# Performance work log

Measured on AMD Instinct MI355X. Metric: run time of the kernel, lower is better.

The kernel has to match this reference:

```python
import jax, jax.numpy as jnp
import numpy as np

N_NODES = 100000
D = 128


def _sage_layer(h, src, dst, w_self, w_neigh, b):
    # GraphSAGE mean aggregation: mean of neighbor (src) features per dst node.
    msg = h[src]                                            # [E, D] gather
    agg = jax.ops.segment_sum(msg, dst, num_segments=N_NODES)  # [N, D]
    deg = jax.ops.segment_sum(jnp.ones(src.shape, h.dtype), dst, num_segments=N_NODES)
    mean = agg / jnp.maximum(deg, 1.0)[:, None]
    return h @ w_self + mean @ w_neigh + b


def setup_inputs() -> dict:
    key = jax.random.key(0)
    ks = jax.random.split(key, 16)
    E = 1600000
    inp = {
        "feat": jax.random.normal(ks[0], (N_NODES, D), jnp.float32),
        "edge0_src": jax.random.randint(ks[1], (E,), 0, N_NODES),
        "edge0_dst": jax.random.randint(ks[2], (E,), 0, N_NODES),
        "edge1_src": jax.random.randint(ks[3], (E,), 0, N_NODES),
        "edge1_dst": jax.random.randint(ks[4], (E,), 0, N_NODES),
        "pos_src": jax.random.randint(ks[5], (100000,), 0, N_NODES),
        "pos_dst": jax.random.randint(ks[6], (100000,), 0, N_NODES),
        "neg_src": jax.random.randint(ks[7], (500000,), 0, N_NODES),
        "neg_dst": jax.random.randint(ks[8], (500000,), 0, N_NODES),
        # learned parameters
        "w_proj": jax.random.normal(ks[9], (D, D), jnp.float32) / np.sqrt(D),
        "b_proj": jnp.zeros((D,), jnp.float32),
        "w_self1": jax.random.normal(ks[10], (D, D), jnp.float32) / np.sqrt(D),
        "w_neigh1": jax.random.normal(ks[11], (D, D), jnp.float32) / np.sqrt(D),
        "b1": jnp.zeros((D,), jnp.float32),
        "w_self2": jax.random.normal(ks[12], (D, D), jnp.float32) / np.sqrt(D),
        "w_neigh2": jax.random.normal(ks[13], (D, D), jnp.float32) / np.sqrt(D),
        "b2": jnp.zeros((D,), jnp.float32),
    }
    return inp


def reference(feat, edge0_src, edge0_dst, edge1_src, edge1_dst,
              pos_src, pos_dst, neg_src, neg_dst,
              w_proj, b_proj, w_self1, w_neigh1, b1, w_self2, w_neigh2, b2):
    # ProjectionLayer: per-node linear + ReLU on blocks[0].srcdata['feature']
    h = jax.nn.relu(feat @ w_proj + b_proj)
    # GNNLayer: one SAGE-mean layer per block
    h = jax.nn.relu(_sage_layer(h, edge0_src, edge0_dst, w_self1, w_neigh1, b1))
    h = _sage_layer(h, edge1_src, edge1_dst, w_self2, w_neigh2, b2)
    # PredictionLayer: dot-product edge scoring on pos_graph / neg_graph
    pos_score = jnp.sum(h[pos_src] * h[pos_dst], axis=-1)
    neg_score = jnp.sum(h[neg_src] * h[neg_dst], axis=-1)
    return (pos_score, neg_score)
```

## Files before the change

### kernel.cpp

```cpp
#include <hip/hip_runtime.h>
#include <hip/hip_bf16.h>

#define NN 100000
#define DD 128

#define NPB 512
#define NB 196
#define CAPB 12288
#define PA_BLOCKS 196
#define GBLK 782

typedef unsigned short ushort_t;
typedef unsigned int uint_t;
typedef __attribute__((ext_vector_type(8))) short bf16x8;
typedef __attribute__((ext_vector_type(4))) float f32x4;

__device__ __forceinline__ ushort_t f2bf(float f) {
    uint_t u = __builtin_bit_cast(uint_t, f);
    u += 0x7FFFu + ((u >> 16) & 1u);
    return (ushort_t)(u >> 16);
}
__device__ __forceinline__ uint_t pack2bf(float a, float b) {
    return (uint_t)f2bf(a) | ((uint_t)f2bf(b) << 16);
}
__device__ __forceinline__ float bflo(uint_t v) {
    return __builtin_bit_cast(float, v << 16);
}
__device__ __forceinline__ float bfhi(uint_t v) {
    return __builtin_bit_cast(float, v & 0xFFFF0000u);
}

__device__ __forceinline__ void gload16(const ushort_t* g, ushort_t* l) {
    __builtin_amdgcn_global_load_lds(
        (const __attribute__((address_space(1))) void*)g,
        (__attribute__((address_space(3))) void*)l,
        16, 0, 0);
}

#define PREP_W_BLOCKS 320
#define PREP_Z_BLOCKS 3
__global__ __launch_bounds__(256) void prep(
    const float* __restrict__ w_proj,
    const float* __restrict__ w_self1, const float* __restrict__ w_neigh1,
    const float* __restrict__ w_self2, const float* __restrict__ w_neigh2,
    ushort_t* __restrict__ wtp, ushort_t* __restrict__ wt1,
    ushort_t* __restrict__ wt2, int* __restrict__ bcnt,
    ushort_t* __restrict__ h1pad, ushort_t* __restrict__ h2pad)
{
    const int bid = blockIdx.x;
    const int tid = threadIdx.x;
    if (bid < PREP_W_BLOCKS) {
        int which = bid >> 6;
        int t = (bid & 63) * 256 + tid;
        int n = t >> 7, k = t & 127;
        float v;
        ushort_t* d;
        switch (which) {
            case 0: v = w_proj  [(size_t)k * 128 + n]; d = wtp + (size_t)n * 128 + k;       break;
            case 1: v = w_self1 [(size_t)k * 128 + n]; d = wt1 + (size_t)n * 256 + k;       break;
            case 2: v = w_neigh1[(size_t)k * 128 + n]; d = wt1 + (size_t)n * 256 + 128 + k; break;
            case 3: v = w_self2 [(size_t)k * 128 + n]; d = wt2 + (size_t)n * 256 + k;       break;
            default:v = w_neigh2[(size_t)k * 128 + n]; d = wt2 + (size_t)n * 256 + 128 + k; break;
        }
        *d = f2bf(v);
    } else if (bid < PREP_W_BLOCKS + 2) {
        int i = (bid - PREP_W_BLOCKS) * 256 + tid;
        if (i < 2 * NB) bcnt[i] = 0;
    } else {
        uint_t* p1 = (uint_t*)h1pad;
        uint_t* p2 = (uint_t*)h2pad;
        if (tid < 64) p1[tid] = 0;
        else if (tid < 128) p2[tid - 64] = 0;
    }
}

__global__ __launch_bounds__(256, 4) void gemm0_partA2(
    const float* __restrict__ feat, const ushort_t* __restrict__ W,
    const float* __restrict__ bias, ushort_t* __restrict__ outp,
    const int* __restrict__ e0s, const int* __restrict__ e0d, int E0,
    const int* __restrict__ e1s, const int* __restrict__ e1d, int E1,
    int* __restrict__ bcnt, uint_t* __restrict__ pairs)
{
    __shared__ char smem[32768];
    const int tid = threadIdx.x;

    if (blockIdx.x < GBLK) {
        ushort_t* At = (ushort_t*)smem;
        ushort_t* Wt = (ushort_t*)(smem + 8192);
        ushort_t* Ot = (ushort_t*)smem;

        const int lane = tid & 63;
        const int wav  = tid >> 6;
        const int row0 = blockIdx.x * 128;
        const int m0   = (wav & 1) * 64;
        const int n0   = (wav >> 1) * 64;

        f32x4 acc[4][4];
#pragma unroll
        for (int i = 0; i < 4; ++i)
#pragma unroll
            for (int j = 0; j < 4; ++j) acc[i][j] = (f32x4){0.f, 0.f, 0.f, 0.f};

        const int cl = lane & 15;
        const int q  = lane >> 4;

#pragma unroll 1
        for (int ch = 0; ch < 4; ++ch) {
            const int kA = ch * 32;

            if (ch) __syncthreads();
#pragma unroll
            for (int j = 0; j < 2; ++j) {
                int cb = (j * 4 + wav) * 64;
                int c  = cb + lane;
                int r  = c >> 2, k2 = c & 3;
                gload16(W + (size_t)r * 128 + kA + k2 * 8, Wt + cb * 8);
            }
            uint4 av[2];
#pragma unroll
            for (int j = 0; j < 2; ++j) {
                int g = tid + 256 * j;
                int r = g >> 2;
                int c = (g & 3) * 8;
                int grow = row0 + r;
                if (grow >= NN) grow = NN - 1;
                float4 f0 = *(const float4*)(feat + (size_t)grow * DD + kA + c);
                float4 f1 = *(const float4*)(feat + (size_t)grow * DD + kA + c + 4);
                av[j].x = pack2bf(f0.x, f0.y);
                av[j].y = pack2bf(f0.z, f0.w);
                av[j].z = pack2bf(f1.x, f1.y);
                av[j].w = pack2bf(f1.z, f1.w);
            }
#pragma unroll
            for (int j = 0; j < 2; ++j) {
                int g = tid + 256 * j;
                int r = g >> 2;
                int c = (g & 3) * 8;
                *(uint4*)(&At[r * 32 + c]) = av[j];
            }
            __syncthreads();

            bf16x8 af[4], bfr[4];
#pragma unroll
            for (int i = 0; i < 4; ++i)
                af[i] = *(const bf16x8*)(&At[(m0 + i * 16 + cl) * 32 + q * 8]);
#pragma unroll
            for (int j = 0; j < 4; ++j)
                bfr[j] = *(const bf16x8*)(&Wt[(n0 + j * 16 + cl) * 32 + q * 8]);
#pragma unroll
            for (int i = 0; i < 4; ++i)
#pragma unroll
                for (int j = 0; j < 4; ++j)
                    acc[i][j] = __builtin_amdgcn_mfma_f32_16x16x32_bf16(
                        af[i], bfr[j], acc[i][j], 0, 0, 0);
        }

        __syncthreads();
#pragma unroll
        for (int j = 0; j < 4; ++j) {
            int c = n0 + j * 16 + cl;
            float bv = bias[c];
#pragma unroll
            for (int i = 0; i < 4; ++i) {
#pragma unroll
                for (int reg = 0; reg < 4; ++reg) {
                    int r = m0 + i * 16 + 4 * q + reg;
                    float v = acc[i][j][reg] + bv;
                    v = fmaxf(v, 0.f);
                    Ot[r * 128 + c] = f2bf(v);
                }
            }
        }
        __syncthreads();
        int rows = NN - row0; if (rows > 128) rows = 128;
        for (int t = tid; t < rows * 16; t += 256) {
            int r = t >> 4, c8 = (t & 15) * 8;
            *(uint4*)(outp + (size_t)(row0 + r) * DD + c8) =
                *(const uint4*)(&Ot[r * 128 + c8]);
        }
    } else {
        int* hist = (int*)smem;
        int* base = (int*)(smem + 1024);

        const int bid  = blockIdx.x - GBLK;
        const int half = bid >= PA_BLOCKS;
        const int* __restrict__ src = half ? e1s : e0s;
        const int* __restrict__ dst = half ? e1d : e0d;
        const int E = half ? E1 : E0;
        int* bc = bcnt + half * NB;
        uint_t* pp = pairs + (size_t)half * NB * CAPB;
        const int blk = bid - half * PA_BLOCKS;
        const int chunk = (E + PA_BLOCKS - 1) / PA_BLOCKS;
        const int ea = blk * chunk;
        int eb = ea + chunk; if (eb > E) eb = E;

        for (int b = tid; b < NB; b += 256) hist[b] = 0;
        __syncthreads();
        for (int e = ea + tid; e < eb; e += 256)
            atomicAdd(&hist[dst[e] >> 9], 1);
        __syncthreads();
        for (int b = tid; b < NB; b += 256) {
            base[b] = atomicAdd(&bc[b], hist[b]);
            hist[b] = 0;
        }
        __syncthreads();
        for (int e = ea + tid; e < eb; e += 256) {
            int d = dst[e];
            int b = d >> 9;
            int off = atomicAdd(&hist[b], 1);
            int p = base[b] + off;
            if (p < CAPB)
                pp[(size_t)b * CAPB + p] =
                    ((uint_t)(d & (NPB - 1)) << 17) | (uint_t)src[e];
        }
    }
}

template <bool RELU>
__global__ __launch_bounds__(256, 4) void gemm_bf16(
    const ushort_t* __restrict__ Av, const ushort_t* __restrict__ Bm,
    const ushort_t* __restrict__ W, const float* __restrict__ bias,
    ushort_t* __restrict__ outp)
{
    __shared__ char smem[32768];
    ushort_t* Ot = (ushort_t*)smem;

    const int tid  = threadIdx.x;
    const int lane = tid & 63;
    const int wav  = tid >> 6;
    const int row0 = blockIdx.x * 128;
    const int m0   = (wav & 1) * 64;
    const int n0   = (wav >> 1) * 64;
    const int KTOT = 256;
    const int NCH  = 8;

    f32x4 acc[4][4];
#pragma unroll
    for (int i = 0; i < 4; ++i)
#pragma unroll
        for (int j = 0; j < 4; ++j) acc[i][j] = (f32x4){0.f, 0.f, 0.f, 0.f};

    const int cl = lane & 15;
    const int q  = lane >> 4;

    auto STAGE = [&](int ch, int buf) {
        const bool second = (ch >= 4);
        const int kA = (ch & 3) * 32;
        const int kW = ch * 32;
        ushort_t* At = (ushort_t*)(smem + buf * 16384);
        ushort_t* Wt = At + 4096;
        const ushort_t* sp = second ? Bm : Av;
#pragma unroll
        for (int j = 0; j < 2; ++j) {
            int cb = (j * 4 + wav) * 64;
            int c  = cb + lane;
            int r  = c >> 2, k2 = c & 3;
            int grow = row0 + r;
            if (grow >= NN) grow = NN - 1;
            gload16(sp + (size_t)grow * DD + kA + k2 * 8, At + cb * 8);
            gload16(W + (size_t)r * KTOT + kW + k2 * 8, Wt + cb * 8);
        }
    };
    auto COMPUTE = [&](int buf) {
        ushort_t* At = (ushort_t*)(smem + buf * 16384);
        ushort_t* Wt = At + 4096;
        bf16x8 af[4], bfr[4];
#pragma unroll
        for (int i = 0; i < 4; ++i)
            af[i] = *(const bf16x8*)(&At[(m0 + i * 16 + cl) * 32 + q * 8]);
#pragma unroll
        for (int j = 0; j < 4; ++j)
            bfr[j] = *(const bf16x8*)(&Wt[(n0 + j * 16 + cl) * 32 + q * 8]);
#pragma unroll
        for (int i = 0; i < 4; ++i)
#pragma unroll
            for (int j = 0; j < 4; ++j)
                acc[i][j] = __builtin_amdgcn_mfma_f32_16x16x32_bf16(
                    af[i], bfr[j], acc[i][j], 0, 0, 0);
    };

    STAGE(0, 0);
    asm volatile("s_waitcnt vmcnt(0)" ::: "memory");
    __builtin_amdgcn_s_barrier();
    int cur = 0;
#pragma unroll 1
    for (int ch = 0; ch < NCH - 1; ++ch) {
        STAGE(ch + 1, cur ^ 1);
        COMPUTE(cur);
        asm volatile("s_waitcnt vmcnt(0)" ::: "memory");
        __builtin_amdgcn_s_barrier();
        cur ^= 1;
    }
    COMPUTE(cur);

    __syncthreads();
#pragma unroll
    for (int j = 0; j < 4; ++j) {
        int c = n0 + j * 16 + cl;
        float bv = bias[c];
#pragma unroll
        for (int i = 0; i < 4; ++i) {
#pragma unroll
            for (int reg = 0; reg < 4; ++reg) {
                int r = m0 + i * 16 + 4 * q + reg;
                float v = acc[i][j][reg] + bv;
                if constexpr (RELU) v = fmaxf(v, 0.f);
                Ot[r * 128 + c] = f2bf(v);
            }
        }
    }
    __syncthreads();
    int rows = NN - row0; if (rows > 128) rows = 128;
    for (int t = tid; t < rows * 16; t += 256) {
        int r = t >> 4, c8 = (t & 15) * 8;
        *(uint4*)(outp + (size_t)(row0 + r) * DD + c8) =
            *(const uint4*)(&Ot[r * 128 + c8]);
    }
}

__global__ __launch_bounds__(256, 2) void partB(
    uint_t* __restrict__ pairs, const int* __restrict__ bcnt,
    int* __restrict__ counts, int* __restrict__ offs)
{
    __shared__ int cnt[NPB];
    __shared__ int loff[NPB];
    __shared__ int ssc[256];
    __shared__ int image[CAPB];

    const int tid  = threadIdx.x;
    const int half = blockIdx.x >= NB;
    const int b    = blockIdx.x - half * NB;
    const int n0   = b << 9;
    int nb = NN - n0; if (nb > NPB) nb = NPB;
    int tot = bcnt[half * NB + b]; if (tot > CAPB) tot = CAPB;
    uint_t* pb = pairs + (size_t)(half * NB + b) * CAPB;
    const int gbase = (half * NB + b) * CAPB;
    int* cnts  = counts + (size_t)half * NN;
    int* offsl = offs   + (size_t)half * NN;

    for (int n = tid; n < NPB; n += 256) cnt[n] = 0;
    __syncthreads();
    for (int i = tid; i < tot; i += 256)
        atomicAdd(&cnt[pb[i] >> 17], 1);
    __syncthreads();

    int a0 = cnt[2 * tid], a1 = cnt[2 * tid + 1];
    int s = a0 + a1;
    ssc[tid] = s;
    __syncthreads();
    for (int off = 1; off < 256; off <<= 1) {
        int t = 0;
        if (tid >= off) t = ssc[tid - off];
        __syncthreads();
        if (tid >= off) ssc[tid] += t;
        __syncthreads();
    }
    int pre = ssc[tid] - s;
    loff[2 * tid]     = pre;
    loff[2 * tid + 1] = pre + a0;
    __syncthreads();

    for (int n = tid; n < nb; n += 256) {
        cnts[n0 + n]  = cnt[n];
        offsl[n0 + n] = gbase + loff[n];
    }
    for (int n = tid; n < NPB; n += 256) cnt[n] = 0;
    __syncthreads();

    for (int i = tid; i < tot; i += 256) {
        uint_t p = pb[i];
        int ln  = p >> 17;
        int pos = loff[ln] + atomicAdd(&cnt[ln], 1);
        image[pos] = (int)(p & 0x1FFFFu);
    }
    __syncthreads();
    for (int i = tid; i < tot; i += 256) pb[i] = (uint_t)image[i];
}

#define AGG_ISSUE(V, J)                                                   \
    do {                                                                  \
        int s_[8];                                                        \
        _Pragma("unroll")                                                 \
        for (int u = 0; u < 8; ++u) {                                     \
            int jj = (J) + u;                                             \
            int jc = jj < cnt ? jj : cnt - 1;                             \
            int sv = (int)csr[start + jc];                                \
            s_[u] = jj < cnt ? sv : NN;                                   \
        }                                                                 \
        _Pragma("unroll")                                                 \
        for (int u = 0; u < 8; ++u)                                       \
            V[u] = *(const uint4*)(hl + (size_t)s_[u] * DD);              \
    } while (0)

#define AGG_ACCUM(V)                                                      \
    do {                                                                  \
        _Pragma("unroll")                                                 \
        for (int u = 0; u < 8; ++u) {                                     \
            a0 += bflo(V[u].x); a1 += bfhi(V[u].x);                       \
            a2 += bflo(V[u].y); a3 += bfhi(V[u].y);                       \
            a4 += bflo(V[u].z); a5 += bfhi(V[u].z);                       \
            a6 += bflo(V[u].w); a7 += bfhi(V[u].w);                       \
        }                                                                 \
    } while (0)

__global__ __launch_bounds__(256) void aggregate_bf16(
    const ushort_t* __restrict__ h, const uint_t* __restrict__ csr,
    const int* __restrict__ offs, const int* __restrict__ counts,
    ushort_t* __restrict__ mean, int nn)
{
    int gid  = blockIdx.x * 256 + threadIdx.x;
    int node = gid >> 4;
    if (node >= nn) return;
    int lane  = gid & 15;
    int start = offs[node];
    int cnt   = counts[node];
    const ushort_t* __restrict__ hl = h + lane * 8;

    float a0 = 0.f, a1 = 0.f, a2 = 0.f, a3 = 0.f;
    float a4 = 0.f, a5 = 0.f, a6 = 0.f, a7 = 0.f;

    int nbt = (cnt + 7) >> 3;
    if (nbt > 0) {
        uint4 va[8], vb[8];
        AGG_ISSUE(va, 0);
        int j = 8, b = 1;
        for (; b + 1 < nbt; b += 2) {
            AGG_ISSUE(vb, j); j += 8;
            AGG_ACCUM(va);
            AGG_ISSUE(va, j); j += 8;
            AGG_ACCUM(vb);
        }
        if (b < nbt) {
            AGG_ISSUE(vb, j);
            AGG_ACCUM(va);
            AGG_ACCUM(vb);
        } else {
            AGG_ACCUM(va);
        }
    }

    float rinv = 1.0f / (float)(cnt > 1 ? cnt : 1);
    uint4 o;
    o.x = pack2bf(a0 * rinv, a1 * rinv);
    o.y = pack2bf(a2 * rinv, a3 * rinv);
    o.z = pack2bf(a4 * rinv, a5 * rinv);
    o.w = pack2bf(a6 * rinv, a7 * rinv);
    *(uint4*)(mean + (size_t)node * DD + lane * 8) = o;
}

__device__ __forceinline__ float dot8(uint4 a, uint4 b) {
    return bflo(a.x) * bflo(b.x) + bfhi(a.x) * bfhi(b.x)
         + bflo(a.y) * bflo(b.y) + bfhi(a.y) * bfhi(b.y)
         + bflo(a.z) * bflo(b.z) + bfhi(a.z) * bfhi(b.z)
         + bflo(a.w) * bflo(b.w) + bfhi(a.w) * bfhi(b.w);
}

__global__ __launch_bounds__(256) void score_both(
    const ushort_t* __restrict__ h,
    const int* __restrict__ ps, const int* __restrict__ pd,
    const int* __restrict__ ns, const int* __restrict__ nd,
    float* __restrict__ out, int EP, int TE)
{
    int gid = blockIdx.x * 256 + threadIdx.x;
    int grp = gid >> 4;
    int e0 = grp * 2;
    if (e0 >= TE) return;
    int lane = gid & 15;
    int e1 = e0 + 1;
    bool has1 = (e1 < TE);
    int ee = has1 ? e1 : e0;

    int s0, d0, s1, d1;
    if (e0 < EP) { s0 = ps[e0]; d0 = pd[e0]; }
    else         { s0 = ns[e0 - EP]; d0 = nd[e0 - EP]; }
    if (ee < EP) { s1 = ps[ee]; d1 = pd[ee]; }
    else         { s1 = ns[ee - EP]; d1 = nd[ee - EP]; }

    const ushort_t* __restrict__ hl = h + lane * 8;
    uint4 va0 = *(const uint4*)(hl + (size_t)s0 * DD);
    uint4 vb0 = *(const uint4*)(hl + (size_t)d0 * DD);
    uint4 va1 = *(const uint4*)(hl + (size_t)s1 * DD);
    uint4 vb1 = *(const uint4*)(hl + (size_t)d1 * DD);

    float r0 = dot8(va0, vb0);
    float r1 = dot8(va1, vb1);
#pragma unroll
    for (int off = 8; off; off >>= 1) {
        r0 += __shfl_down(r0, off, 16);
        r1 += __shfl_down(r1, off, 16);
    }
    if (lane == 0) {
        out[e0] = r0;
        if (has1) out[e1] = r1;
    }
}


extern "C" void kernel_launch(void* const* d_in, const int* in_sizes, int n_in,
                              void* d_out, int out_size, void* d_ws, size_t ws_size,
                              hipStream_t stream)
{
    const float* feat    = (const float*)d_in[0];
    const int*   e0s     = (const int*)d_in[1];
    const int*   e0d     = (const int*)d_in[2];
    const int*   e1s     = (const int*)d_in[3];
    const int*   e1d     = (const int*)d_in[4];
    const int*   ps      = (const int*)d_in[5];
    const int*   pd      = (const int*)d_in[6];
    const int*   ns      = (const int*)d_in[7];
    const int*   nd      = (const int*)d_in[8];
    const float* w_proj  = (const float*)d_in[9];
    const float* b_proj  = (const float*)d_in[10];
    const float* w_self1 = (const float*)d_in[11];
    const float* w_neigh1= (const float*)d_in[12];
    const float* b1      = (const float*)d_in[13];
    const float* w_self2 = (const float*)d_in[14];
    const float* w_neigh2= (const float*)d_in[15];
    const float* b2      = (const float*)d_in[16];

    float* out = (float*)d_out;

    const size_t NF  = (size_t)NN * DD;
    const size_t NFP = NF + DD;
    char* base = (char*)d_ws;

    ushort_t* h3   = (ushort_t*)base;
    ushort_t* h1   = h3 + NFP;
    ushort_t* mean = h1 + NFP;
    ushort_t* h2   = mean + NFP;

    uint_t* pairs  = (uint_t*)(h2 + NFP);
    int*    bcnt   = (int*)(pairs + (size_t)2 * NB * CAPB);
    int*    counts = bcnt + 2 * NB;
    int*    offs   = counts + 2 * NN;
    ushort_t* wts  = (ushort_t*)(offs + 2 * NN);
    ushort_t* wtp = wts;
    ushort_t* wt1 = wts + 128 * 128;
    ushort_t* wt2 = wt1 + 128 * 256;

    const int E0 = in_sizes[1];
    const int E1 = in_sizes[3];
    const int EP = in_sizes[5];
    const int EN = in_sizes[7];

    const int AGB = (NN * 16 + 255) / 256;

    prep<<<PREP_W_BLOCKS + PREP_Z_BLOCKS, 256, 0, stream>>>(
        w_proj, w_self1, w_neigh1, w_self2, w_neigh2, wtp, wt1, wt2, bcnt,
        h1 + NF, h2 + NF);

    gemm0_partA2<<<GBLK + 2 * PA_BLOCKS, 256, 0, stream>>>(
        feat, wtp, b_proj, h1, e0s, e0d, E0, e1s, e1d, E1, bcnt, pairs);

    partB<<<2 * NB, 256, 0, stream>>>(pairs, bcnt, counts, offs);

    aggregate_bf16<<<AGB, 256, 0, stream>>>(h1, pairs, offs, counts, mean, NN);
    gemm_bf16<true><<<GBLK, 256, 0, stream>>>(h1, mean, wt1, b1, h2);

    aggregate_bf16<<<AGB, 256, 0, stream>>>(
        h2, pairs, offs + NN, counts + NN, mean, NN);
    gemm_bf16<false><<<GBLK, 256, 0, stream>>>(h2, mean, wt2, b2, h3);

    const int TE = EP + EN;
    const int NG = (TE + 1) / 2;
    score_both<<<(NG * 16 + 255) / 256, 256, 0, stream>>>(
        h3, ps, pd, ns, nd, out, EP, TE);
}
```

Before: 402.7 us.

## Fuse neighbor mean aggregation into SAGE layer GEMM via shared-memory mean tile

Each SAGE layer now runs as one kernel. Every 128-row block first gathers and averages neighbor features for its nodes into a padded shared-memory tile, then runs the concatenated self/neighbor GEMM using that tile directly. This removes the global round trip of the mean buffer and two kernel launches. The projection GEMM and edge bucketing are also split back into separate kernels. In exchange, the GEMM loses its double-buffered staging, shared memory per block rises to about 50KB, and occupancy is capped at 3 blocks, so gather latency can no longer be hidden by as many resident waves.

```diff
diff --git a/kernel.cpp b/kernel.cpp
--- a/kernel.cpp
+++ b/kernel.cpp
@@ -74,155 +74,13 @@
     }
 }
 
-__global__ __launch_bounds__(256, 4) void gemm0_partA2(
+__global__ __launch_bounds__(256, 4) void gemm0(
     const float* __restrict__ feat, const ushort_t* __restrict__ W,
-    const float* __restrict__ bias, ushort_t* __restrict__ outp,
-    const int* __restrict__ e0s, const int* __restrict__ e0d, int E0,
-    const int* __restrict__ e1s, const int* __restrict__ e1d, int E1,
-    int* __restrict__ bcnt, uint_t* __restrict__ pairs)
+    const float* __restrict__ bias, ushort_t* __restrict__ outp)
 {
     __shared__ char smem[32768];
-    const int tid = threadIdx.x;
-
-    if (blockIdx.x < GBLK) {
-        ushort_t* At = (ushort_t*)smem;
-        ushort_t* Wt = (ushort_t*)(smem + 8192);
-        ushort_t* Ot = (ushort_t*)smem;
-
-        const int lane = tid & 63;
-        const int wav  = tid >> 6;
-        const int row0 = blockIdx.x * 128;
-        const int m0   = (wav & 1) * 64;
-        const int n0   = (wav >> 1) * 64;
-
-        f32x4 acc[4][4];
-#pragma unroll
-        for (int i = 0; i < 4; ++i)
-#pragma unroll
-            for (int j = 0; j < 4; ++j) acc[i][j] = (f32x4){0.f, 0.f, 0.f, 0.f};
-
-        const int cl = lane & 15;
-        const int q  = lane >> 4;
-
-#pragma unroll 1
-        for (int ch = 0; ch < 4; ++ch) {
-            const int kA = ch * 32;
-
-            if (ch) __syncthreads();
-#pragma unroll
-            for (int j = 0; j < 2; ++j) {
-                int cb = (j * 4 + wav) * 64;
-                int c  = cb + lane;
-                int r  = c >> 2, k2 = c & 3;
-                gload16(W + (size_t)r * 128 + kA + k2 * 8, Wt + cb * 8);
-            }
-            uint4 av[2];
-#pragma unroll
-            for (int j = 0; j < 2; ++j) {
-                int g = tid + 256 * j;
-                int r = g >> 2;
-                int c = (g & 3) * 8;
-                int grow = row0 + r;
-                if (grow >= NN) grow = NN - 1;
-                float4 f0 = *(const float4*)(feat + (size_t)grow * DD + kA + c);
-                float4 f1 = *(const float4*)(feat + (size_t)grow * DD + kA + c + 4);
-                av[j].x = pack2bf(f0.x, f0.y);
-                av[j].y = pack2bf(f0.z, f0.w);
-                av[j].z = pack2bf(f1.x, f1.y);
-                av[j].w = pack2bf(f1.z, f1.w);
-            }
-#pragma unroll
-            for (int j = 0; j < 2; ++j) {
-                int g = tid + 256 * j;
-                int r = g >> 2;
-                int c = (g & 3) * 8;
-                *(uint4*)(&At[r * 32 + c]) = av[j];
-            }
-            __syncthreads();
-
-            bf16x8 af[4], bfr[4];
-#pragma unroll
-            for (int i = 0; i < 4; ++i)
-                af[i] = *(const bf16x8*)(&At[(m0 + i * 16 + cl) * 32 + q * 8]);
-#pragma unroll
-            for (int j = 0; j < 4; ++j)
-                bfr[j] = *(const bf16x8*)(&Wt[(n0 + j * 16 + cl) * 32 + q * 8]);
-#pragma unroll
-            for (int i = 0; i < 4; ++i)
-#pragma unroll
-                for (int j = 0; j < 4; ++j)
-                    acc[i][j] = __builtin_amdgcn_mfma_f32_16x16x32_bf16(
-                        af[i], bfr[j], acc[i][j], 0, 0, 0);
-        }
-
-        __syncthreads();
-#pragma unroll
-        for (int j = 0; j < 4; ++j) {
-            int c = n0 + j * 16 + cl;
-            float bv = bias[c];
-#pragma unroll
-            for (int i = 0; i < 4; ++i) {
-#pragma unroll
-                for (int reg = 0; reg < 4; ++reg) {
-                    int r = m0 + i * 16 + 4 * q + reg;
-                    float v = acc[i][j][reg] + bv;
-                    v = fmaxf(v, 0.f);
-                    Ot[r * 128 + c] = f2bf(v);
-                }
-            }
-        }
-        __syncthreads();
-        int rows = NN - row0; if (rows > 128) rows = 128;
-        for (int t = tid; t < rows * 16; t += 256) {
-            int r = t >> 4, c8 = (t & 15) * 8;
-            *(uint4*)(outp + (size_t)(row0 + r) * DD + c8) =
-                *(const uint4*)(&Ot[r * 128 + c8]);
-        }
-    } else {
-        int* hist = (int*)smem;
-        int* base = (int*)(smem + 1024);
-
-        const int bid  = blockIdx.x - GBLK;
-        const int half = bid >= PA_BLOCKS;
-        const int* __restrict__ src = half ? e1s : e0s;
-        const int* __restrict__ dst = half ? e1d : e0d;
-        const int E = half ? E1 : E0;
-        int* bc = bcnt + half * NB;
-        uint_t* pp = pairs + (size_t)half * NB * CAPB;
-        const int blk = bid - half * PA_BLOCKS;
-        const int chunk = (E + PA_BLOCKS - 1) / PA_BLOCKS;
-        const int ea = blk * chunk;
-        int eb = ea + chunk; if (eb > E) eb = E;
-
-        for (int b = tid; b < NB; b += 256) hist[b] = 0;
-        __syncthreads();
-        for (int e = ea + tid; e < eb; e += 256)
-            atomicAdd(&hist[dst[e] >> 9], 1);
-        __syncthreads();
-        for (int b = tid; b < NB; b += 256) {
-            base[b] = atomicAdd(&bc[b], hist[b]);
-            hist[b] = 0;
-        }
-        __syncthreads();
-        for (int e = ea + tid; e < eb; e += 256) {
-            int d = dst[e];
-            int b = d >> 9;
-            int off = atomicAdd(&hist[b], 1);
-            int p = base[b] + off;
-            if (p < CAPB)
-                pp[(size_t)b * CAPB + p] =
-                    ((uint_t)(d & (NPB - 1)) << 17) | (uint_t)src[e];
-        }
-    }
-}
-
-template <bool RELU>
-__global__ __launch_bounds__(256, 4) void gemm_bf16(
-    const ushort_t* __restrict__ Av, const ushort_t* __restrict__ Bm,
-    const ushort_t* __restrict__ W, const float* __restrict__ bias,
-    ushort_t* __restrict__ outp)
-{
-    __shared__ char smem[32768];
+    ushort_t* At = (ushort_t*)smem;
+    ushort_t* Wt = (ushort_t*)(smem + 8192);
     ushort_t* Ot = (ushort_t*)smem;
 
     const int tid  = threadIdx.x;
@@ -231,8 +89,6 @@
     const int row0 = blockIdx.x * 128;
     const int m0   = (wav & 1) * 64;
     const int n0   = (wav >> 1) * 64;
-    const int KTOT = 256;
-    const int NCH  = 8;
 
     f32x4 acc[4][4];
 #pragma unroll
@@ -243,27 +99,42 @@
     const int cl = lane & 15;
     const int q  = lane >> 4;
 
-    auto STAGE = [&](int ch, int buf) {
-        const bool second = (ch >= 4);
-        const int kA = (ch & 3) * 32;
-        const int kW = ch * 32;
-        ushort_t* At = (ushort_t*)(smem + buf * 16384);
-        ushort_t* Wt = At + 4096;
-        const ushort_t* sp = second ? Bm : Av;
+#pragma unroll 1
+    for (int ch = 0; ch < 4; ++ch) {
+        const int kA = ch * 32;
+
+        if (ch) __syncthreads();
 #pragma unroll
         for (int j = 0; j < 2; ++j) {
             int cb = (j * 4 + wav) * 64;
             int c  = cb + lane;
             int r  = c >> 2, k2 = c & 3;
+            gload16(W + (size_t)r * 128 + kA + k2 * 8, Wt + cb * 8);
+        }
+        uint4 av[2];
+#pragma unroll
+        for (int j = 0; j < 2; ++j) {
+            int g = tid + 256 * j;
+            int r = g >> 2;
+            int c = (g & 3) * 8;
             int grow = row0 + r;
             if (grow >= NN) grow = NN - 1;
-            gload16(sp + (size_t)grow * DD + kA + k2 * 8, At + cb * 8);
-            gload16(W + (size_t)r * KTOT + kW + k2 * 8, Wt + cb * 8);
-        }
-    };
-    auto COMPUTE = [&](int buf) {
-        ushort_t* At = (ushort_t*)(smem + buf * 16384);
-        ushort_t* Wt = At + 4096;
+            float4 f0 = *(const float4*)(feat + (size_t)grow * DD + kA + c);
+            float4 f1 = *(const float4*)(feat + (size_t)grow * DD + kA + c + 4);
+            av[j].x = pack2bf(f0.x, f0.y);
+            av[j].y = pack2bf(f0.z, f0.w);
+            av[j].z = pack2bf(f1.x, f1.y);
+            av[j].w = pack2bf(f1.z, f1.w);
+        }
+#pragma unroll
+        for (int j = 0; j < 2; ++j) {
+            int g = tid + 256 * j;
+            int r = g >> 2;
+            int c = (g & 3) * 8;
+            *(uint4*)(&At[r * 32 + c]) = av[j];
+        }
+        __syncthreads();
+
         bf16x8 af[4], bfr[4];
 #pragma unroll
         for (int i = 0; i < 4; ++i)
@@ -277,21 +148,7 @@
             for (int j = 0; j < 4; ++j)
                 acc[i][j] = __builtin_amdgcn_mfma_f32_16x16x32_bf16(
                     af[i], bfr[j], acc[i][j], 0, 0, 0);
-    };
-
-    STAGE(0, 0);
-    asm volatile("s_waitcnt vmcnt(0)" ::: "memory");
-    __builtin_amdgcn_s_barrier();
-    int cur = 0;
-#pragma unroll 1
-    for (int ch = 0; ch < NCH - 1; ++ch) {
-        STAGE(ch + 1, cur ^ 1);
-        COMPUTE(cur);
-        asm volatile("s_waitcnt vmcnt(0)" ::: "memory");
-        __builtin_amdgcn_s_barrier();
-        cur ^= 1;
-    }
-    COMPUTE(cur);
+    }
 
     __syncthreads();
 #pragma unroll
@@ -304,7 +161,7 @@
             for (int reg = 0; reg < 4; ++reg) {
                 int r = m0 + i * 16 + 4 * q + reg;
                 float v = acc[i][j][reg] + bv;
-                if constexpr (RELU) v = fmaxf(v, 0.f);
+                v = fmaxf(v, 0.f);
                 Ot[r * 128 + c] = f2bf(v);
             }
         }
@@ -315,6 +172,46 @@
         int r = t >> 4, c8 = (t & 15) * 8;
         *(uint4*)(outp + (size_t)(row0 + r) * DD + c8) =
             *(const uint4*)(&Ot[r * 128 + c8]);
+    }
+}
+
+__global__ __launch_bounds__(256) void partA2(
+    const int* __restrict__ e0s, const int* __restrict__ e0d, int E0,
+    const int* __restrict__ e1s, const int* __restrict__ e1d, int E1,
+    int* __restrict__ bcnt, uint_t* __restrict__ pairs)
+{
+    __shared__ int hist[NB];
+    __shared__ int base[NB];
+    const int tid  = threadIdx.x;
+    const int half = blockIdx.x >= PA_BLOCKS;
+    const int* __restrict__ src = half ? e1s : e0s;
+    const int* __restrict__ dst = half ? e1d : e0d;
+    const int E = half ? E1 : E0;
+    int* bc = bcnt + half * NB;
+    uint_t* pp = pairs + (size_t)half * NB * CAPB;
+    const int blk = blockIdx.x - half * PA_BLOCKS;
+    const int chunk = (E + PA_BLOCKS - 1) / PA_BLOCKS;
+    const int ea = blk * chunk;
+    int eb = ea + chunk; if (eb > E) eb = E;
+
+    for (int b = tid; b < NB; b += 256) hist[b] = 0;
+    __syncthreads();
+    for (int e = ea + tid; e < eb; e += 256)
+        atomicAdd(&hist[dst[e] >> 9], 1);
+    __syncthreads();
+    for (int b = tid; b < NB; b += 256) {
+        base[b] = atomicAdd(&bc[b], hist[b]);
+        hist[b] = 0;
+    }
+    __syncthreads();
+    for (int e = ea + tid; e < eb; e += 256) {
+        int d = dst[e];
+        int b = d >> 9;
+        int off = atomicAdd(&hist[b], 1);
+        int p = base[b] + off;
+        if (p < CAPB)
+            pp[(size_t)b * CAPB + p] =
+                ((uint_t)(d & (NPB - 1)) << 17) | (uint_t)src[e];
     }
 }
 
@@ -403,49 +300,163 @@
         }                                                                 \
     } while (0)
 
-__global__ __launch_bounds__(256) void aggregate_bf16(
-    const ushort_t* __restrict__ h, const uint_t* __restrict__ csr,
+template <bool RELU>
+__global__ __launch_bounds__(256, 3) void fused_layer(
+    const ushort_t* __restrict__ hin, const uint_t* __restrict__ csr,
     const int* __restrict__ offs, const int* __restrict__ counts,
-    ushort_t* __restrict__ mean, int nn)
-{
-    int gid  = blockIdx.x * 256 + threadIdx.x;
-    int node = gid >> 4;
-    if (node >= nn) return;
-    int lane  = gid & 15;
-    int start = offs[node];
-    int cnt   = counts[node];
-    const ushort_t* __restrict__ hl = h + lane * 8;
-
-    float a0 = 0.f, a1 = 0.f, a2 = 0.f, a3 = 0.f;
-    float a4 = 0.f, a5 = 0.f, a6 = 0.f, a7 = 0.f;
-
-    int nbt = (cnt + 7) >> 3;
-    if (nbt > 0) {
-        uint4 va[8], vb[8];
-        AGG_ISSUE(va, 0);
-        int j = 8, b = 1;
-        for (; b + 1 < nbt; b += 2) {
-            AGG_ISSUE(vb, j); j += 8;
-            AGG_ACCUM(va);
-            AGG_ISSUE(va, j); j += 8;
-            AGG_ACCUM(vb);
-        }
-        if (b < nbt) {
-            AGG_ISSUE(vb, j);
-            AGG_ACCUM(va);
-            AGG_ACCUM(vb);
-        } else {
-            AGG_ACCUM(va);
-        }
-    }
-
-    float rinv = 1.0f / (float)(cnt > 1 ? cnt : 1);
-    uint4 o;
-    o.x = pack2bf(a0 * rinv, a1 * rinv);
-    o.y = pack2bf(a2 * rinv, a3 * rinv);
-    o.z = pack2bf(a4 * rinv, a5 * rinv);
-    o.w = pack2bf(a6 * rinv, a7 * rinv);
-    *(uint4*)(mean + (size_t)node * DD + lane * 8) = o;
+    const ushort_t* __restrict__ W, const float* __restrict__ bias,
+    ushort_t* __restrict__ outp)
+{
+    __shared__ char smem[51200];
+    ushort_t* Mean = (ushort_t*)smem;
+    ushort_t* Wt   = (ushort_t*)(smem + 34816);
+    ushort_t* At   = (ushort_t*)(smem + 43008);
+    ushort_t* Ot   = (ushort_t*)smem;
+
+    const int tid  = threadIdx.x;
+    const int row0 = blockIdx.x * 128;
+
+    {
+        const int grp    = tid >> 4;
+        const int lane16 = tid & 15;
+        const ushort_t* __restrict__ hl = hin + lane16 * 8;
+#pragma unroll 1
+        for (int g = 0; g < 8; ++g) {
+            int nloc = g * 16 + grp;
+            int node = row0 + nloc;
+            if (node >= NN) node = NN - 1;
+            int start = offs[node];
+            int cnt   = counts[node];
+
+            float a0 = 0.f, a1 = 0.f, a2 = 0.f, a3 = 0.f;
+            float a4 = 0.f, a5 = 0.f, a6 = 0.f, a7 = 0.f;
+            int nbt = (cnt + 7) >> 3;
+            if (nbt > 0) {
+                uint4 va[8], vb[8];
+                AGG_ISSUE(va, 0);
+                int j = 8, b = 1;
+                for (; b + 1 < nbt; b += 2) {
+                    AGG_ISSUE(vb, j); j += 8;
+                    AGG_ACCUM(va);
+                    AGG_ISSUE(va, j); j += 8;
+                    AGG_ACCUM(vb);
+                }
+                if (b < nbt) {
+                    AGG_ISSUE(vb, j);
+                    AGG_ACCUM(va);
+                    AGG_ACCUM(vb);
+                } else {
+                    AGG_ACCUM(va);
+                }
+            }
+            float rinv = 1.0f / (float)(cnt > 1 ? cnt : 1);
+            uint4 o;
+            o.x = pack2bf(a0 * rinv, a1 * rinv);
+            o.y = pack2bf(a2 * rinv, a3 * rinv);
+            o.z = pack2bf(a4 * rinv, a5 * rinv);
+            o.w = pack2bf(a6 * rinv, a7 * rinv);
+            *(uint4*)(&Mean[nloc * 136 + lane16 * 8]) = o;
+        }
+    }
+
+    const int lane = tid & 63;
+    const int wav  = tid >> 6;
+    const int m0   = (wav & 1) * 64;
+    const int n0   = (wav >> 1) * 64;
+    const int cl   = lane & 15;
+    const int q    = lane >> 4;
+
+    f32x4 acc[4][4];
+#pragma unroll
+    for (int i = 0; i < 4; ++i)
+#pragma unroll
+        for (int j = 0; j < 4; ++j) acc[i][j] = (f32x4){0.f, 0.f, 0.f, 0.f};
+
+    __syncthreads();
+
+#pragma unroll 1
+    for (int ch = 4; ch < 8; ++ch) {
+        const int kA = (ch & 3) * 32;
+        const int kW = ch * 32;
+        if (ch > 4) __syncthreads();
+#pragma unroll
+        for (int j = 0; j < 2; ++j) {
+            int cb = (j * 4 + wav) * 64;
+            int c  = cb + lane;
+            int r  = c >> 2, k2 = c & 3;
+            gload16(W + (size_t)r * 256 + kW + k2 * 8, Wt + cb * 8);
+        }
+        __syncthreads();
+
+        bf16x8 af[4], bfr[4];
+#pragma unroll
+        for (int i = 0; i < 4; ++i)
+            af[i] = *(const bf16x8*)(&Mean[(m0 + i * 16 + cl) * 136 + kA + q * 8]);
+#pragma unroll
+        for (int j = 0; j < 4; ++j)
+            bfr[j] = *(const bf16x8*)(&Wt[(n0 + j * 16 + cl) * 32 + q * 8]);
+#pragma unroll
+        for (int i = 0; i < 4; ++i)
+#pragma unroll
+            for (int j = 0; j < 4; ++j)
+                acc[i][j] = __builtin_amdgcn_mfma_f32_16x16x32_bf16(
+                    af[i], bfr[j], acc[i][j], 0, 0, 0);
+    }
+
+#pragma unroll 1
+    for (int ch = 0; ch < 4; ++ch) {
+        const int kA = ch * 32;
+        __syncthreads();
+#pragma unroll
+        for (int j = 0; j < 2; ++j) {
+            int cb = (j * 4 + wav) * 64;
+            int c  = cb + lane;
+            int r  = c >> 2, k2 = c & 3;
+            int grow = row0 + r;
+            if (grow >= NN) grow = NN - 1;
+            gload16(hin + (size_t)grow * DD + kA + k2 * 8, At + cb * 8);
+            gload16(W + (size_t)r * 256 + kA + k2 * 8, Wt + cb * 8);
+        }
+        __syncthreads();
+
+        bf16x8 af[4], bfr[4];
+#pragma unroll
+        for (int i = 0; i < 4; ++i)
+            af[i] = *(const bf16x8*)(&At[(m0 + i * 16 + cl) * 32 + q * 8]);
+#pragma unroll
+        for (int j = 0; j < 4; ++j)
+            bfr[j] = *(const bf16x8*)(&Wt[(n0 + j * 16 + cl) * 32 + q * 8]);
+#pragma unroll
+        for (int i = 0; i < 4; ++i)
+#pragma unroll
+            for (int j = 0; j < 4; ++j)
+                acc[i][j] = __builtin_amdgcn_mfma_f32_16x16x32_bf16(
+                    af[i], bfr[j], acc[i][j], 0, 0, 0);
+    }
+
+    __syncthreads();
+#pragma unroll
+    for (int j = 0; j < 4; ++j) {
+        int c = n0 + j * 16 + cl;
+        float bv = bias[c];
+#pragma unroll
+        for (int i = 0; i < 4; ++i) {
+#pragma unroll
+            for (int reg = 0; reg < 4; ++reg) {
+                int r = m0 + i * 16 + 4 * q + reg;
+                float v = acc[i][j][reg] + bv;
+                if constexpr (RELU) v = fmaxf(v, 0.f);
+                Ot[r * 128 + c] = f2bf(v);
+            }
+        }
+    }
+    __syncthreads();
+    int rows = NN - row0; if (rows > 128) rows = 128;
+    for (int t = tid; t < rows * 16; t += 256) {
+        int r = t >> 4, c8 = (t & 15) * 8;
+        *(uint4*)(outp + (size_t)(row0 + r) * DD + c8) =
+            *(const uint4*)(&Ot[r * 128 + c8]);
+    }
 }
 
 __device__ __forceinline__ float dot8(uint4 a, uint4 b) {
@@ -543,23 +554,21 @@
     const int EP = in_sizes[5];
     const int EN = in_sizes[7];
 
-    const int AGB = (NN * 16 + 255) / 256;
-
     prep<<<PREP_W_BLOCKS + PREP_Z_BLOCKS, 256, 0, stream>>>(
         w_proj, w_self1, w_neigh1, w_self2, w_neigh2, wtp, wt1, wt2, bcnt,
         h1 + NF, h2 + NF);
 
-    gemm0_partA2<<<GBLK + 2 * PA_BLOCKS, 256, 0, stream>>>(
-        feat, wtp, b_proj, h1, e0s, e0d, E0, e1s, e1d, E1, bcnt, pairs);
-
+    partA2<<<2 * PA_BLOCKS, 256, 0, stream>>>(
+        e0s, e0d, E0, e1s, e1d, E1, bcnt, pairs);
     partB<<<2 * NB, 256, 0, stream>>>(pairs, bcnt, counts, offs);
 
-    aggregate_bf16<<<AGB, 256, 0, stream>>>(h1, pairs, offs, counts, mean, NN);
-    gemm_bf16<true><<<GBLK, 256, 0, stream>>>(h1, mean, wt1, b1, h2);
-
-    aggregate_bf16<<<AGB, 256, 0, stream>>>(
-        h2, pairs, offs + NN, counts + NN, mean, NN);
-    gemm_bf16<false><<<GBLK, 256, 0, stream>>>(h2, mean, wt2, b2, h3);
+    gemm0<<<GBLK, 256, 0, stream>>>(feat, wtp, b_proj, h1);
+
+    fused_layer<true><<<GBLK, 256, 0, stream>>>(
+        h1, pairs, offs, counts, wt1, b1, h2);
+
+    fused_layer<false><<<GBLK, 256, 0, stream>>>(
+        h2, pairs, offs + NN, counts + NN, wt2, b2, h3);
 
     const int TE = EP + EN;
     const int NG = (TE + 1) / 2;
```

Result: slower. 422.5 us (+4.9%).

## Split fused projection GEMM and edge bucketing into separate kernels with 512-thread blocks

Applied to the files above, without the earlier changes.

The combined gemm0_partA2 launch is split into a standalone projection GEMM and a standalone edge-bucketing kernel. partA2 and partB now run with 512-thread blocks, and partB's scan works on one element per thread. The projection GEMM is launched after partB so the bucketing work no longer shares a grid with the GEMM. This trades the overlap that came from fusing the two jobs for simpler, better-occupied kernels, at the cost of an extra kernel launch.

```diff
diff --git a/kernel.cpp b/kernel.cpp
--- a/kernel.cpp
+++ b/kernel.cpp
@@ -74,146 +74,201 @@
     }
 }
 
-__global__ __launch_bounds__(256, 4) void gemm0_partA2(
+__global__ __launch_bounds__(256, 4) void gemm0(
     const float* __restrict__ feat, const ushort_t* __restrict__ W,
-    const float* __restrict__ bias, ushort_t* __restrict__ outp,
+    const float* __restrict__ bias, ushort_t* __restrict__ outp)
+{
+    __shared__ char smem[32768];
+    ushort_t* At = (ushort_t*)smem;
+    ushort_t* Wt = (ushort_t*)(smem + 8192);
+    ushort_t* Ot = (ushort_t*)smem;
+
+    const int tid  = threadIdx.x;
+    const int lane = tid & 63;
+    const int wav  = tid >> 6;
+    const int row0 = blockIdx.x * 128;
+    const int m0   = (wav & 1) * 64;
+    const int n0   = (wav >> 1) * 64;
+
+    f32x4 acc[4][4];
+#pragma unroll
+    for (int i = 0; i < 4; ++i)
+#pragma unroll
+        for (int j = 0; j < 4; ++j) acc[i][j] = (f32x4){0.f, 0.f, 0.f, 0.f};
+
+    const int cl = lane & 15;
+    const int q  = lane >> 4;
+
+#pragma unroll 1
+    for (int ch = 0; ch < 4; ++ch) {
+        const int kA = ch * 32;
+
+        if (ch) __syncthreads();
+#pragma unroll
+        for (int j = 0; j < 2; ++j) {
+            int cb = (j * 4 + wav) * 64;
+            int c  = cb + lane;
+            int r  = c >> 2, k2 = c & 3;
+            gload16(W + (size_t)r * 128 + kA + k2 * 8, Wt + cb * 8);
+        }
+        uint4 av[2];
+#pragma unroll
+        for (int j = 0; j < 2; ++j) {
+            int g = tid + 256 * j;
+            int r = g >> 2;
+            int c = (g & 3) * 8;
+            int grow = row0 + r;
+            if (grow >= NN) grow = NN - 1;
+            float4 f0 = *(const float4*)(feat + (size_t)grow * DD + kA + c);
+            float4 f1 = *(const float4*)(feat + (size_t)grow * DD + kA + c + 4);
+            av[j].x = pack2bf(f0.x, f0.y);
+            av[j].y = pack2bf(f0.z, f0.w);
+            av[j].z = pack2bf(f1.x, f1.y);
+            av[j].w = pack2bf(f1.z, f1.w);
+        }
+#pragma unroll
+        for (int j = 0; j < 2; ++j) {
+            int g = tid + 256 * j;
+            int r = g >> 2;
+            int c = (g & 3) * 8;
+            *(uint4*)(&At[r * 32 + c]) = av[j];
+        }
+        __syncthreads();
+
+        bf16x8 af[4], bfr[4];
+#pragma unroll
+        for (int i = 0; i < 4; ++i)
+            af[i] = *(const bf16x8*)(&At[(m0 + i * 16 + cl) * 32 + q * 8]);
+#pragma unroll
+        for (int j = 0; j < 4; ++j)
+            bfr[j] = *(const bf16x8*)(&Wt[(n0 + j * 16 + cl) * 32 + q * 8]);
+#pragma unroll
+        for (int i = 0; i < 4; ++i)
+#pragma unroll
+            for (int j = 0; j < 4; ++j)
+                acc[i][j] = __builtin_amdgcn_mfma_f32_16x16x32_bf16(
+                    af[i], bfr[j], acc[i][j], 0, 0, 0);
+    }
+
+    __syncthreads();
+#pragma unroll
+    for (int j = 0; j < 4; ++j) {
+        int c = n0 + j * 16 + cl;
+        float bv = bias[c];
+#pragma unroll
+        for (int i = 0; i < 4; ++i) {
+#pragma unroll
+            for (int reg = 0; reg < 4; ++reg) {
+                int r = m0 + i * 16 + 4 * q + reg;
+                float v = acc[i][j][reg] + bv;
+                v = fmaxf(v, 0.f);
+                Ot[r * 128 + c] = f2bf(v);
+            }
+        }
+    }
+    __syncthreads();
+    int rows = NN - row0; if (rows > 128) rows = 128;
+    for (int t = tid; t < rows * 16; t += 256) {
+        int r = t >> 4, c8 = (t & 15) * 8;
+        *(uint4*)(outp + (size_t)(row0 + r) * DD + c8) =
+            *(const uint4*)(&Ot[r * 128 + c8]);
+    }
+}
+
+__global__ __launch_bounds__(512) void partA2(
     const int* __restrict__ e0s, const int* __restrict__ e0d, int E0,
     const int* __restrict__ e1s, const int* __restrict__ e1d, int E1,
     int* __restrict__ bcnt, uint_t* __restrict__ pairs)
 {
-    __shared__ char smem[32768];
-    const int tid = threadIdx.x;
-
-    if (blockIdx.x < GBLK) {
-        ushort_t* At = (ushort_t*)smem;
-        ushort_t* Wt = (ushort_t*)(smem + 8192);
-        ushort_t* Ot = (ushort_t*)smem;
-
-        const int lane = tid & 63;
-        const int wav  = tid >> 6;
-        const int row0 = blockIdx.x * 128;
-        const int m0   = (wav & 1) * 64;
-        const int n0   = (wav >> 1) * 64;
-
-        f32x4 acc[4][4];
-#pragma unroll
-        for (int i = 0; i < 4; ++i)
-#pragma unroll
-            for (int j = 0; j < 4; ++j) acc[i][j] = (f32x4){0.f, 0.f, 0.f, 0.f};
-
-        const int cl = lane & 15;
-        const int q  = lane >> 4;
-
-#pragma unroll 1
-        for (int ch = 0; ch < 4; ++ch) {
-            const int kA = ch * 32;
-
-            if (ch) __syncthreads();
-#pragma unroll
-            for (int j = 0; j < 2; ++j) {
-                int cb = (j * 4 + wav) * 64;
-                int c  = cb + lane;
-                int r  = c >> 2, k2 = c & 3;
-                gload16(W + (size_t)r * 128 + kA + k2 * 8, Wt + cb * 8);
-            }
-            uint4 av[2];
-#pragma unroll
-            for (int j = 0; j < 2; ++j) {
-                int g = tid + 256 * j;
-                int r = g >> 2;
-                int c = (g & 3) * 8;
-                int grow = row0 + r;
-                if (grow >= NN) grow = NN - 1;
-                float4 f0 = *(const float4*)(feat + (size_t)grow * DD + kA + c);
-                float4 f1 = *(const float4*)(feat + (size_t)grow * DD + kA + c + 4);
-                av[j].x = pack2bf(f0.x, f0.y);
-                av[j].y = pack2bf(f0.z, f0.w);
-                av[j].z = pack2bf(f1.x, f1.y);
-                av[j].w = pack2bf(f1.z, f1.w);
-            }
-#pragma unroll
-            for (int j = 0; j < 2; ++j) {
-                int g = tid + 256 * j;
-                int r = g >> 2;
-                int c = (g & 3) * 8;
-                *(uint4*)(&At[r * 32 + c]) = av[j];
-            }
-            __syncthreads();
-
-            bf16x8 af[4], bfr[4];
-#pragma unroll
-            for (int i = 0; i < 4; ++i)
-                af[i] = *(const bf16x8*)(&At[(m0 + i * 16 + cl) * 32 + q * 8]);
-#pragma unroll
-            for (int j = 0; j < 4; ++j)
-                bfr[j] = *(const bf16x8*)(&Wt[(n0 + j * 16 + cl) * 32 + q * 8]);
-#pragma unroll
-            for (int i = 0; i < 4; ++i)
-#pragma unroll
-                for (int j = 0; j < 4; ++j)
-                    acc[i][j] = __builtin_amdgcn_mfma_f32_16x16x32_bf16(
-                        af[i], bfr[j], acc[i][j], 0, 0, 0);
-        }
-
+    __shared__ int hist[NB];
+    __shared__ int base[NB];
+    const int tid  = threadIdx.x;
+    const int half = blockIdx.x >= PA_BLOCKS;
+    const int* __restrict__ src = half ? e1s : e0s;
+    const int* __restrict__ dst = half ? e1d : e0d;
+    const int E = half ? E1 : E0;
+    int* bc = bcnt + half * NB;
+    uint_t* pp = pairs + (size_t)half * NB * CAPB;
+    const int blk = blockIdx.x - half * PA_BLOCKS;
+    const int chunk = (E + PA_BLOCKS - 1) / PA_BLOCKS;
+    const int ea = blk * chunk;
+    int eb = ea + chunk; if (eb > E) eb = E;
+
+    for (int b = tid; b < NB; b += 512) hist[b] = 0;
+    __syncthreads();
+    for (int e = ea + tid; e < eb; e += 512)
+        atomicAdd(&hist[dst[e] >> 9], 1);
+    __syncthreads();
+    for (int b = tid; b < NB; b += 512) {
+        base[b] = atomicAdd(&bc[b], hist[b]);
+        hist[b] = 0;
+    }
+    __syncthreads();
+    for (int e = ea + tid; e < eb; e += 512) {
+        int d = dst[e];
+        int b = d >> 9;
+        int off = atomicAdd(&hist[b], 1);
+        int p = base[b] + off;
+        if (p < CAPB)
+            pp[(size_t)b * CAPB + p] =
+                ((uint_t)(d & (NPB - 1)) << 17) | (uint_t)src[e];
+    }
+}
+
+__global__ __launch_bounds__(512) void partB(
+    uint_t* __restrict__ pairs, const int* __restrict__ bcnt,
+    int* __restrict__ counts, int* __restrict__ offs)
+{
+    __shared__ int cnt[NPB];
+    __shared__ int loff[NPB];
+    __shared__ int ssc[NPB];
+    __shared__ int image[CAPB];
+
+    const int tid  = threadIdx.x;
+    const int half = blockIdx.x >= NB;
+    const int b    = blockIdx.x - half * NB;
+    const int n0   = b << 9;
+    int nb = NN - n0; if (nb > NPB) nb = NPB;
+    int tot = bcnt[half * NB + b]; if (tot > CAPB) tot = CAPB;
+    uint_t* pb = pairs + (size_t)(half * NB + b) * CAPB;
+    const int gbase = (half * NB + b) * CAPB;
+    int* cnts  = counts + (size_t)half * NN;
+    int* offsl = offs   + (size_t)half * NN;
+
+    cnt[tid] = 0;
+    __syncthreads();
+    for (int i = tid; i < tot; i += 512)
+        atomicAdd(&cnt[pb[i] >> 17], 1);
+    __syncthreads();
+
+    int s = cnt[tid];
+    ssc[tid] = s;
+    __syncthreads();
+    for (int off = 1; off < NPB; off <<= 1) {
+        int t = 0;
+        if (tid >= off) t = ssc[tid - off];
         __syncthreads();
-#pragma unroll
-        for (int j = 0; j < 4; ++j) {
-            int c = n0 + j * 16 + cl;
-            float bv = bias[c];
-#pragma unroll
-            for (int i = 0; i < 4; ++i) {
-#pragma unroll
-                for (int reg = 0; reg < 4; ++reg) {
-                    int r = m0 + i * 16 + 4 * q + reg;
-                    float v = acc[i][j][reg] + bv;
-                    v = fmaxf(v, 0.f);
-                    Ot[r * 128 + c] = f2bf(v);
-                }
-            }
-        }
+        if (tid >= off) ssc[tid] += t;
         __syncthreads();
-        int rows = NN - row0; if (rows > 128) rows = 128;
-        for (int t = tid; t < rows * 16; t += 256) {
-            int r = t >> 4, c8 = (t & 15) * 8;
-            *(uint4*)(outp + (size_t)(row0 + r) * DD + c8) =
-                *(const uint4*)(&Ot[r * 128 + c8]);
-        }
-    } else {
-        int* hist = (int*)smem;
-        int* base = (int*)(smem + 1024);
-
-        const int bid  = blockIdx.x - GBLK;
-        const int half = bid >= PA_BLOCKS;
-        const int* __restrict__ src = half ? e1s : e0s;
-        const int* __restrict__ dst = half ? e1d : e0d;
-        const int E = half ? E1 : E0;
-        int* bc = bcnt + half * NB;
-        uint_t* pp = pairs + (size_t)half * NB * CAPB;
-        const int blk = bid - half * PA_BLOCKS;
-        const int chunk = (E + PA_BLOCKS - 1) / PA_BLOCKS;
-        const int ea = blk * chunk;
-        int eb = ea + chunk; if (eb > E) eb = E;
-
-        for (int b = tid; b < NB; b += 256) hist[b] = 0;
-        __syncthreads();
-        for (int e = ea + tid; e < eb; e += 256)
-            atomicAdd(&hist[dst[e] >> 9], 1);
-        __syncthreads();
-        for (int b = tid; b < NB; b += 256) {
-            base[b] = atomicAdd(&bc[b], hist[b]);
-            hist[b] = 0;
-        }
-        __syncthreads();
-        for (int e = ea + tid; e < eb; e += 256) {
-            int d = dst[e];
-            int b = d >> 9;
-            int off = atomicAdd(&hist[b], 1);
-            int p = base[b] + off;
-            if (p < CAPB)
-                pp[(size_t)b * CAPB + p] =
-                    ((uint_t)(d & (NPB - 1)) << 17) | (uint_t)src[e];
-        }
-    }
+    }
+    loff[tid] = ssc[tid] - s;
+    __syncthreads();
+
+    if (tid < nb) {
+        cnts[n0 + tid]  = cnt[tid];
+        offsl[n0 + tid] = gbase + loff[tid];
+    }
+    cnt[tid] = 0;
+    __syncthreads();
+
+    for (int i = tid; i < tot; i += 512) {
+        uint_t p = pb[i];
+        int ln  = p >> 17;
+        int pos = loff[ln] + atomicAdd(&cnt[ln], 1);
+        image[pos] = (int)(p & 0x1FFFFu);
+    }
+    __syncthreads();
+    for (int i = tid; i < tot; i += 512) pb[i] = (uint_t)image[i];
 }
 
 template <bool RELU>
@@ -316,65 +371,6 @@
         *(uint4*)(outp + (size_t)(row0 + r) * DD + c8) =
             *(const uint4*)(&Ot[r * 128 + c8]);
     }
-}
-
-__global__ __launch_bounds__(256, 2) void partB(
-    uint_t* __restrict__ pairs, const int* __restrict__ bcnt,
-    int* __restrict__ counts, int* __restrict__ offs)
-{
-    __shared__ int cnt[NPB];
-    __shared__ int loff[NPB];
-    __shared__ int ssc[256];
-    __shared__ int image[CAPB];
-
-    const int tid  = threadIdx.x;
-    const int half = blockIdx.x >= NB;
-    const int b    = blockIdx.x - half * NB;
-    const int n0   = b << 9;
-    int nb = NN - n0; if (nb > NPB) nb = NPB;
-    int tot = bcnt[half * NB + b]; if (tot > CAPB) tot = CAPB;
-    uint_t* pb = pairs + (size_t)(half * NB + b) * CAPB;
-    const int gbase = (half * NB + b) * CAPB;
-    int* cnts  = counts + (size_t)half * NN;
-    int* offsl = offs   + (size_t)half * NN;
-
-    for (int n = tid; n < NPB; n += 256) cnt[n] = 0;
-    __syncthreads();
-    for (int i = tid; i < tot; i += 256)
-        atomicAdd(&cnt[pb[i] >> 17], 1);
-    __syncthreads();
-
-    int a0 = cnt[2 * tid], a1 = cnt[2 * tid + 1];
-    int s = a0 + a1;
-    ssc[tid] = s;
-    __syncthreads();
-    for (int off = 1; off < 256; off <<= 1) {
-        int t = 0;
-        if (tid >= off) t = ssc[tid - off];
-        __syncthreads();
-        if (tid >= off) ssc[tid] += t;
-        __syncthreads();
-    }
-    int pre = ssc[tid] - s;
-    loff[2 * tid]     = pre;
-    loff[2 * tid + 1] = pre + a0;
-    __syncthreads();
-
-    for (int n = tid; n < nb; n += 256) {
-        cnts[n0 + n]  = cnt[n];
-        offsl[n0 + n] = gbase + loff[n];
-    }
-    for (int n = tid; n < NPB; n += 256) cnt[n] = 0;
-    __syncthreads();
-
-    for (int i = tid; i < tot; i += 256) {
-        uint_t p = pb[i];
-        int ln  = p >> 17;
-        int pos = loff[ln] + atomicAdd(&cnt[ln], 1);
-        image[pos] = (int)(p & 0x1FFFFu);
-    }
-    __syncthreads();
-    for (int i = tid; i < tot; i += 256) pb[i] = (uint_t)image[i];
 }
 
 #define AGG_ISSUE(V, J)                                                   \
@@ -549,10 +545,11 @@
         w_proj, w_self1, w_neigh1, w_self2, w_neigh2, wtp, wt1, wt2, bcnt,
         h1 + NF, h2 + NF);
 
-    gemm0_partA2<<<GBLK + 2 * PA_BLOCKS, 256, 0, stream>>>(
-        feat, wtp, b_proj, h1, e0s, e0d, E0, e1s, e1d, E1, bcnt, pairs);
-
-    partB<<<2 * NB, 256, 0, stream>>>(pairs, bcnt, counts, offs);
+    partA2<<<2 * PA_BLOCKS, 512, 0, stream>>>(
+        e0s, e0d, E0, e1s, e1d, E1, bcnt, pairs);
+    partB<<<2 * NB, 512, 0, stream>>>(pairs, bcnt, counts, offs);
+
+    gemm0<<<GBLK, 256, 0, stream>>>(feat, wtp, b_proj, h1);
 
     aggregate_bf16<<<AGB, 256, 0, stream>>>(h1, pairs, offs, counts, mean, NN);
     gemm_bf16<true><<<GBLK, 256, 0, stream>>>(h1, mean, wt1, b1, h2);
```

Result: faster. 387.7 us (-3.7%).
